# Kernel optimization log

Hardware: AMD Instinct MI355X
Metric: run time of the kernel (lower is better)

Reference implementation:

```python
import jax, jax.numpy as jnp
import numpy as np

B, DIN, H, DOUT = 2048, 1024, 2048, 1024
N_WIDTH, N_ROUTED = 8, 4  # n_layers - 2 = 4 routed expert layers
BN_EPS = 1e-5


def setup_inputs() -> dict:
    key = jax.random.key(0)
    ks = jax.random.split(key, 8)
    # kaiming-normal-ish scales
    x = jax.random.normal(ks[0], (B, DIN), dtype=jnp.float32)
    start_W = jax.random.normal(ks[1], (DIN, H), dtype=jnp.float32) * np.sqrt(2.0 / DIN)
    start_b = jnp.zeros((H,), jnp.float32)
    start_gamma = jnp.ones((H,), jnp.float32)
    start_beta = jnp.zeros((H,), jnp.float32)
    expert_W = jax.random.normal(ks[2], (N_ROUTED, N_WIDTH, H, H), dtype=jnp.float32) * np.sqrt(2.0 / H)
    expert_b = jnp.zeros((N_ROUTED, N_WIDTH, H), jnp.float32)
    bn_gamma = jnp.ones((N_ROUTED, H), jnp.float32)
    bn_beta = jnp.zeros((N_ROUTED, H), jnp.float32)
    dqn_W = jax.random.normal(ks[3], (H, N_WIDTH), dtype=jnp.float32) * np.sqrt(1.0 / H)
    dqn_b = jnp.zeros((N_WIDTH,), jnp.float32)
    end_W = jax.random.normal(ks[4], (H, DOUT), dtype=jnp.float32) * np.sqrt(2.0 / H)
    end_b = jnp.zeros((DOUT,), jnp.float32)
    return {"x": x, "start_W": start_W, "start_b": start_b,
            "start_gamma": start_gamma, "start_beta": start_beta,
            "expert_W": expert_W, "expert_b": expert_b,
            "bn_gamma": bn_gamma, "bn_beta": bn_beta,
            "dqn_W": dqn_W, "dqn_b": dqn_b,
            "end_W": end_W, "end_b": end_b}


def _batchnorm(h, gamma, beta):
    # training-mode BatchNorm1d: biased variance over batch axis
    mu = h.mean(0)
    var = jnp.mean((h - mu) ** 2, axis=0)
    return gamma * (h - mu) * jax.lax.rsqrt(var + BN_EPS) + beta


def reference(x, start_W, start_b, start_gamma, start_beta,
              expert_W, expert_b, bn_gamma, bn_beta,
              dqn_W, dqn_b, end_W, end_b):
    # start: Linear + ReLU + BatchNorm1d
    h = jax.nn.relu(x @ start_W + start_b)            # [B, H]
    h = _batchnorm(h, start_gamma, start_beta)
    # routed expert layers (eval mode: deterministic argmax routing, eps=-1)
    for i in range(N_ROUTED):
        logits = h @ dqn_W + dqn_b                    # [B, E]
        actions = jnp.argmax(logits, axis=1)          # [B]
        onehot = jax.nn.one_hot(actions, N_WIDTH, dtype=h.dtype)  # [B, E]
        # compute all experts densely, then select per-sample expert
        y_all = jax.nn.relu(jnp.einsum('bi,eio->beo', h, expert_W[i]) + expert_b[i][None])  # [B, E, H]
        h = jnp.einsum('beo,be->bo', y_all, onehot)   # [B, H]
        h = _batchnorm(h, bn_gamma[i], bn_beta[i])
    # end: Linear + ReLU
    return jax.nn.relu(h @ end_W + end_b)             # [B, DOUT]
```

## Files before the change

kernel.cpp:

```cpp
#include <hip/hip_runtime.h>
#include <math.h>

#define B_SZ 2048
#define DIN  1024
#define H    2048
#define DOUT 1024
#define NEXP 8
#define NL   4

typedef _Float16 f16;
typedef _Float16 f16x4 __attribute__((ext_vector_type(4)));
typedef _Float16 f16x8 __attribute__((ext_vector_type(8)));
typedef __fp16   h16x2 __attribute__((ext_vector_type(2)));
typedef float    f32x4 __attribute__((ext_vector_type(4)));

#define MFMA16(a,b,c) __builtin_amdgcn_mfma_f32_16x16x32_f16((a),(b),(c),0,0,0)

__global__ __launch_bounds__(256) void k_convert(const float* __restrict__ x,
                                                 f16* __restrict__ hi, f16* __restrict__ lo, int n4){
  int stride = gridDim.x * blockDim.x;
  for (int i = blockIdx.x*blockDim.x + threadIdx.x; i < n4; i += stride){
    float4 v = ((const float4*)x)[i];
    f16 h0=(f16)v.x, h1=(f16)v.y, h2=(f16)v.z, h3=(f16)v.w;
    f16x4 hv = {h0,h1,h2,h3};
    f16x4 lv = {(f16)((v.x-(float)h0)*2048.0f),(f16)((v.y-(float)h1)*2048.0f),
                (f16)((v.z-(float)h2)*2048.0f),(f16)((v.w-(float)h3)*2048.0f)};
    ((f16x4*)hi)[i] = hv;
    ((f16x4*)lo)[i] = lv;
  }
}

template<int PRECISE>
__global__ __launch_bounds__(256, 2) void k_gemm(
    const f16* __restrict__ Ahi, const f16* __restrict__ Alo, int lda,
    const float* __restrict__ Wbase, const float* __restrict__ biasBase,
    int K, int N, int M, int nTx,
    float* __restrict__ Cout, int ldc,
    const int* __restrict__ row_idx, const int* __restrict__ offsets,
    const int* __restrict__ tile_map, const int* __restrict__ ntiles,
    int wStride, int bStride)
{
  const int q = gridDim.x >> 3;
  const int logical = (blockIdx.x & 7) * q + (blockIdx.x >> 3);
  const int ntile_x = logical % nTx;
  const int mtile_l = logical / nTx;

  const bool ident = (tile_map == nullptr);
  int e, mt, roff, cnt;
  if (!ident){
    if (mtile_l >= *ntiles) return;
    int mv = tile_map[mtile_l]; e = mv >> 16; mt = mv & 0xffff;
    roff = offsets[e]; cnt = offsets[e+1] - roff;
  } else { e = 0; mt = mtile_l; roff = 0; cnt = M; }

  const float* W    = Wbase   + (size_t)e * wStride;
  const float* bias = biasBase+ (size_t)e * bStride;
  const int n0   = ntile_x * 128;
  const int tid  = threadIdx.x;
  const int lane = tid & 63;
  const int wid  = tid >> 6;
  const int wm   = (wid >> 1) * 64;
  const int wn   = (wid & 1) * 64;

  __shared__ f16x8 sAh[128*5];
  __shared__ f16x8 sAl[PRECISE ? 128*5 : 1];
  __shared__ f16x8 sBh[128*5];
  __shared__ f16x8 sBl[PRECISE ? 128*5 : 1];

  const int r1 = tid >> 2, sl = tid & 3, r2 = r1 + 64;
  int gr1, gr2;
  {
    int i1 = mt*128 + r1, i2 = mt*128 + r2;
    if (ident){ gr1 = i1; gr2 = i2; }
    else { gr1 = row_idx[roff + (i1 < cnt ? i1 : 0)];
           gr2 = row_idx[roff + (i2 < cnt ? i2 : 0)]; }
  }
  const f16* a1h = Ahi + (size_t)gr1*lda + sl*8;
  const f16* a2h = Ahi + (size_t)gr2*lda + sl*8;
  const f16 *a1l = nullptr, *a2l = nullptr;
  if constexpr (PRECISE){
    a1l = Alo + (size_t)gr1*lda + sl*8;
    a2l = Alo + (size_t)gr2*lda + sl*8;
  }

  const int bn = tid & 127, kb = tid >> 7;
  const float* wp0 = W + (size_t)(kb*16) * N + n0 + bn;

  f32x4 acc0[4][4] = {};
  f32x4 acc1[4][4] = {};

  f16x8 rA1h, rA2h, rA1l, rA2l;
  float rW[16];

  auto issue = [&](int kk){
    rA1h = *(const f16x8*)(a1h + kk);
    rA2h = *(const f16x8*)(a2h + kk);
    if constexpr (PRECISE){
      rA1l = *(const f16x8*)(a1l + kk);
      rA2l = *(const f16x8*)(a2l + kk);
    }
    const float* wp = wp0 + (size_t)kk * N;
    #pragma unroll
    for (int i = 0; i < 16; i++) rW[i] = wp[(size_t)i * N];
  };

  issue(0);

  for (int k0 = 0; k0 < K; k0 += 32){
    sAh[r1*5 + sl] = rA1h;
    sAh[r2*5 + sl] = rA2h;
    if constexpr (PRECISE){
      sAl[r1*5 + sl] = rA1l;
      sAl[r2*5 + sl] = rA2l;
    }
    {
      f16 hs[16], ls[16];
      #pragma unroll
      for (int i = 0; i < 16; i += 2){
        float w0 = rW[i]   * 16.0f;
        float w1 = rW[i+1] * 16.0f;
        h16x2 hp = __builtin_amdgcn_cvt_pkrtz(w0, w1);
        hs[i] = (f16)hp.x; hs[i+1] = (f16)hp.y;
        if constexpr (PRECISE){
          h16x2 lp = __builtin_amdgcn_cvt_pkrtz((w0-(float)hp.x)*2048.0f,
                                                (w1-(float)hp.y)*2048.0f);
          ls[i] = (f16)lp.x; ls[i+1] = (f16)lp.y;
        }
      }
      f16x8 v0 = {hs[0],hs[1],hs[2],hs[3],hs[4],hs[5],hs[6],hs[7]};
      f16x8 v1 = {hs[8],hs[9],hs[10],hs[11],hs[12],hs[13],hs[14],hs[15]};
      sBh[bn*5 + kb*2 + 0] = v0;
      sBh[bn*5 + kb*2 + 1] = v1;
      if constexpr (PRECISE){
        f16x8 u0 = {ls[0],ls[1],ls[2],ls[3],ls[4],ls[5],ls[6],ls[7]};
        f16x8 u1 = {ls[8],ls[9],ls[10],ls[11],ls[12],ls[13],ls[14],ls[15]};
        sBl[bn*5 + kb*2 + 0] = u0;
        sBl[bn*5 + kb*2 + 1] = u1;
      }
    }
    __syncthreads();

    if (k0 + 32 < K) issue(k0 + 32);

    f16x8 ah[4], al[4];
    #pragma unroll
    for (int mf = 0; mf < 4; mf++){
      int row = wm + mf*16 + (lane & 15);
      ah[mf] = sAh[row*5 + (lane >> 4)];
      if constexpr (PRECISE) al[mf] = sAl[row*5 + (lane >> 4)];
    }
    #pragma unroll
    for (int nf = 0; nf < 4; nf++){
      int col = wn + nf*16 + (lane & 15);
      f16x8 bh = sBh[col*5 + (lane >> 4)];
      f16x8 bl;
      if constexpr (PRECISE) bl = sBl[col*5 + (lane >> 4)];
      #pragma unroll
      for (int mf = 0; mf < 4; mf++){
        acc0[mf][nf] = MFMA16(ah[mf], bh, acc0[mf][nf]);
        if constexpr (PRECISE){
          acc1[mf][nf] = MFMA16(ah[mf], bl, acc1[mf][nf]);
          acc1[mf][nf] = MFMA16(al[mf], bh, acc1[mf][nf]);
        }
      }
    }
    __syncthreads();
  }

  const float s1 = 1.0f/16.0f, s2 = 1.0f/(16.0f*2048.0f);
  float bvs[4];
  #pragma unroll
  for (int nf = 0; nf < 4; nf++) bvs[nf] = bias[n0 + wn + nf*16 + (lane & 15)];
  #pragma unroll
  for (int mf = 0; mf < 4; mf++){
    #pragma unroll
    for (int j = 0; j < 4; j++){
      int rt   = wm + mf*16 + (lane >> 4)*4 + j;
      int ridx = mt*128 + rt;
      int gr; bool valid;
      if (ident){ gr = ridx; valid = true; }
      else { valid = (ridx < cnt); gr = valid ? row_idx[roff + ridx] : 0; }
      if (valid){
        float* cp = Cout + (size_t)gr*ldc + n0 + wn + (lane & 15);
        #pragma unroll
        for (int nf = 0; nf < 4; nf++){
          float v = acc0[mf][nf][j]*s1 + bvs[nf];
          if constexpr (PRECISE) v += acc1[mf][nf][j]*s2;
          v = v > 0.0f ? v : 0.0f;
          cp[nf*16] = v;
        }
      }
    }
  }
}

__global__ __launch_bounds__(256) void k_stats(const float* __restrict__ P,
                                               float* __restrict__ psum, float* __restrict__ psq){
  int c  = blockIdx.x*64 + (threadIdx.x & 63);
  int rs = threadIdx.x >> 6;
  int r0 = blockIdx.y * 256;
  float s = 0.f, q = 0.f;
  for (int r = r0 + rs; r < r0 + 256; r += 4){
    float v = P[(size_t)r*H + c]; s += v; q += v*v;
  }
  __shared__ float ls[4][64], lq[4][64];
  ls[rs][threadIdx.x & 63] = s; lq[rs][threadIdx.x & 63] = q;
  __syncthreads();
  if (threadIdx.x < 64){
    int cc = threadIdx.x;
    float S = ls[0][cc]+ls[1][cc]+ls[2][cc]+ls[3][cc];
    float Q = lq[0][cc]+lq[1][cc]+lq[2][cc]+lq[3][cc];
    psum[(size_t)blockIdx.y*H + blockIdx.x*64 + cc] = S;
    psq [(size_t)blockIdx.y*H + blockIdx.x*64 + cc] = Q;
  }
}

__global__ __launch_bounds__(256) void k_norm(const float* __restrict__ P,
    const float* __restrict__ psum, const float* __restrict__ psq,
    const float* __restrict__ gamma, const float* __restrict__ beta,
    f16* __restrict__ Hhi, f16* __restrict__ Hlo){
  __shared__ float sS[64], sT[64];
  int c0 = blockIdx.x * 64;
  int tid = threadIdx.x;
  if (tid < 64){
    float s = 0.f, q = 0.f;
    #pragma unroll
    for (int j = 0; j < 8; j++){ s += psum[(size_t)j*H + c0 + tid]; q += psq[(size_t)j*H + c0 + tid]; }
    float mu  = s * (1.0f/B_SZ);
    float var = q * (1.0f/B_SZ) - mu*mu; var = var > 0.f ? var : 0.f;
    float r   = 1.0f / sqrtf(var + 1e-5f);
    float g   = gamma[c0 + tid] * r;
    sS[tid] = g; sT[tid] = beta[c0 + tid] - mu*g;
  }
  __syncthreads();
  int cg = (tid & 15) * 4;
  int r0 = blockIdx.y * 256;
  for (int r = r0 + (tid >> 4); r < r0 + 256; r += 16){
    float4 v = *(const float4*)&P[(size_t)r*H + c0 + cg];
    float h0 = v.x*sS[cg]   + sT[cg];
    float h1 = v.y*sS[cg+1] + sT[cg+1];
    float h2 = v.z*sS[cg+2] + sT[cg+2];
    float h3 = v.w*sS[cg+3] + sT[cg+3];
    f16 a0=(f16)h0, a1=(f16)h1, a2=(f16)h2, a3=(f16)h3;
    f16x4 hv = {a0,a1,a2,a3};
    f16x4 lv = {(f16)((h0-(float)a0)*2048.0f),(f16)((h1-(float)a1)*2048.0f),
                (f16)((h2-(float)a2)*2048.0f),(f16)((h3-(float)a3)*2048.0f)};
    *(f16x4*)&Hhi[(size_t)r*H + c0 + cg] = hv;
    *(f16x4*)&Hlo[(size_t)r*H + c0 + cg] = lv;
  }
}

__global__ __launch_bounds__(256) void k_logits(const f16* __restrict__ Hhi, const f16* __restrict__ Hlo,
    const float* __restrict__ dqnW, const float* __restrict__ dqnB, int* __restrict__ actions){
  int row  = blockIdx.x*4 + (threadIdx.x >> 6);
  int lane = threadIdx.x & 63;
  float acc[8] = {0,0,0,0,0,0,0,0};
  const f16* ph = Hhi + (size_t)row*H;
  const f16* pl = Hlo + (size_t)row*H;
  #pragma unroll
  for (int t = 0; t < 4; t++){
    int k = t*512 + lane*8;
    f16x8 h8 = *(const f16x8*)(ph + k);
    f16x8 l8 = *(const f16x8*)(pl + k);
    #pragma unroll
    for (int j = 0; j < 8; j++){
      float h = (float)h8[j] + (float)l8[j]*(1.0f/2048.0f);
      const float* w = dqnW + (size_t)(k+j)*NEXP;
      float4 w0 = *(const float4*)w;
      float4 w1 = *(const float4*)(w+4);
      acc[0] += h*w0.x; acc[1] += h*w0.y; acc[2] += h*w0.z; acc[3] += h*w0.w;
      acc[4] += h*w1.x; acc[5] += h*w1.y; acc[6] += h*w1.z; acc[7] += h*w1.w;
    }
  }
  #pragma unroll
  for (int off = 32; off; off >>= 1){
    #pragma unroll
    for (int e2 = 0; e2 < 8; e2++) acc[e2] += __shfl_down(acc[e2], off);
  }
  if (lane == 0){
    float best = acc[0] + dqnB[0]; int bi = 0;
    #pragma unroll
    for (int e2 = 1; e2 < 8; e2++){ float v = acc[e2] + dqnB[e2]; if (v > best){ best = v; bi = e2; } }
    actions[row] = bi;
  }
}

__global__ __launch_bounds__(256) void k_route(const int* __restrict__ actions, int* __restrict__ offsets,
    int* __restrict__ row_idx, int* __restrict__ tile_map, int* __restrict__ ntiles){
  __shared__ int cnt[8], cur[8];
  int tid = threadIdx.x;
  if (tid < 8) cnt[tid] = 0;
  __syncthreads();
  for (int b = tid; b < B_SZ; b += 256) atomicAdd(&cnt[actions[b]], 1);
  __syncthreads();
  if (tid == 0){
    int o = 0, nt = 0;
    for (int e2 = 0; e2 < 8; e2++){
      offsets[e2] = o; cur[e2] = o;
      int c = cnt[e2];
      int t = (c + 127) >> 7;
      for (int ti = 0; ti < t; ti++) tile_map[nt++] = (e2 << 16) | ti;
      o += c;
    }
    offsets[8] = o;
    *ntiles = nt;
  }
  __syncthreads();
  for (int b = tid; b < B_SZ; b += 256){
    int a = actions[b];
    int p = atomicAdd(&cur[a], 1);
    row_idx[p] = b;
  }
}

extern "C" void kernel_launch(void* const* d_in, const int* in_sizes, int n_in,
                              void* d_out, int out_size, void* d_ws, size_t ws_size,
                              hipStream_t stream){
  const float* x           = (const float*)d_in[0];
  const float* start_W     = (const float*)d_in[1];
  const float* start_b     = (const float*)d_in[2];
  const float* start_gamma = (const float*)d_in[3];
  const float* start_beta  = (const float*)d_in[4];
  const float* expert_W    = (const float*)d_in[5];
  const float* expert_b    = (const float*)d_in[6];
  const float* bn_gamma    = (const float*)d_in[7];
  const float* bn_beta     = (const float*)d_in[8];
  const float* dqn_W       = (const float*)d_in[9];
  const float* dqn_b       = (const float*)d_in[10];
  const float* end_W       = (const float*)d_in[11];
  const float* end_b       = (const float*)d_in[12];
  float* out = (float*)d_out;

  char* ws = (char*)d_ws;
  size_t off = 0;
  auto alloc = [&](size_t bytes){ void* p = ws + off; off += (bytes + 255) & ~(size_t)255; return p; };
  f16*   Hhi     = (f16*)  alloc((size_t)B_SZ*H*2);
  f16*   Hlo     = (f16*)  alloc((size_t)B_SZ*H*2);
  float* Ppre    = (float*)alloc((size_t)B_SZ*H*4);
  float* psum    = (float*)alloc((size_t)8*H*4);
  float* psq     = (float*)alloc((size_t)8*H*4);
  int*   actions = (int*)  alloc(B_SZ*4);
  int*   row_idx = (int*)  alloc(B_SZ*4);
  int*   offsets = (int*)  alloc(16*4);
  int*   tile_map= (int*)  alloc(32*4);
  int*   ntiles  = (int*)  alloc(64);

  k_convert<<<512, 256, 0, stream>>>(x, Hhi, Hlo, B_SZ*DIN/4);
  k_gemm<1><<<(B_SZ/128)*(H/128), 256, 0, stream>>>(
      Hhi, Hlo, DIN, start_W, start_b, DIN, H, B_SZ, H/128, Ppre, H,
      nullptr, nullptr, nullptr, nullptr, 0, 0);
  k_stats<<<dim3(H/64, 8), 256, 0, stream>>>(Ppre, psum, psq);
  k_norm <<<dim3(H/64, 8), 256, 0, stream>>>(Ppre, psum, psq, start_gamma, start_beta, Hhi, Hlo);

  for (int i = 0; i < NL; i++){
    k_logits<<<B_SZ/4, 256, 0, stream>>>(Hhi, Hlo, dqn_W, dqn_b, actions);
    k_route <<<1, 256, 0, stream>>>(actions, offsets, row_idx, tile_map, ntiles);
    const float* Wb = expert_W + (size_t)i*NEXP*H*H;
    const float* bb = expert_b + (size_t)i*NEXP*H;
    if (i < 3)
      k_gemm<1><<<23*(H/128), 256, 0, stream>>>(
          Hhi, Hlo, H, Wb, bb, H, H, B_SZ, H/128, Ppre, H,
          row_idx, offsets, tile_map, ntiles, H*H, H);
    else
      k_gemm<0><<<23*(H/128), 256, 0, stream>>>(
          Hhi, nullptr, H, Wb, bb, H, H, B_SZ, H/128, Ppre, H,
          row_idx, offsets, tile_map, ntiles, H*H, H);
    k_stats<<<dim3(H/64, 8), 256, 0, stream>>>(Ppre, psum, psq);
    k_norm <<<dim3(H/64, 8), 256, 0, stream>>>(Ppre, psum, psq,
        bn_gamma + (size_t)i*H, bn_beta + (size_t)i*H, Hhi, Hlo);
  }

  k_gemm<0><<<(B_SZ/128)*(DOUT/128), 256, 0, stream>>>(
      Hhi, nullptr, H, end_W, end_b, H, DOUT, B_SZ, DOUT/128, out, DOUT,
      nullptr, nullptr, nullptr, nullptr, 0, 0);
}
```

Measured before the change: 742.5 us.

## Double-buffer LDS tiles and deepen weight register prefetch in GEMM

Splits the GEMM main loop into two LDS buffers with two register sets for the fp32 weight tile, so weights are prefetched two k-steps ahead and one barrier per step replaces two. Barriers now wait only on LDS counters, which lets global loads stay in flight across compute. The occupancy hint of 2 blocks per SM is dropped from launch bounds. This doubles LDS use and raises register pressure, which may lower occupancy or cause spills. Correctness relies on K being a multiple of 64 and on the double-buffer ordering of writes against the other buffer's reads.

After: 926.1 us. 1.25x slower.

```diff
diff --git a/kernel.cpp b/kernel.cpp
--- a/kernel.cpp
+++ b/kernel.cpp
@@ -15,6 +15,11 @@
 typedef float    f32x4 __attribute__((ext_vector_type(4)));
 
 #define MFMA16(a,b,c) __builtin_amdgcn_mfma_f32_16x16x32_f16((a),(b),(c),0,0,0)
+
+#define BARRIER_LDS() do { \
+    asm volatile("s_waitcnt lgkmcnt(0)" ::: "memory"); \
+    __builtin_amdgcn_s_barrier(); \
+  } while (0)
 
 __global__ __launch_bounds__(256) void k_convert(const float* __restrict__ x,
                                                  f16* __restrict__ hi, f16* __restrict__ lo, int n4){
@@ -31,7 +36,7 @@
 }
 
 template<int PRECISE>
-__global__ __launch_bounds__(256, 2) void k_gemm(
+__global__ __launch_bounds__(256) void k_gemm(
     const f16* __restrict__ Ahi, const f16* __restrict__ Alo, int lda,
     const float* __restrict__ Wbase, const float* __restrict__ biasBase,
     int K, int N, int M, int nTx,
@@ -62,10 +67,10 @@
   const int wm   = (wid >> 1) * 64;
   const int wn   = (wid & 1) * 64;
 
-  __shared__ f16x8 sAh[128*5];
-  __shared__ f16x8 sAl[PRECISE ? 128*5 : 1];
-  __shared__ f16x8 sBh[128*5];
-  __shared__ f16x8 sBl[PRECISE ? 128*5 : 1];
+  __shared__ f16x8 sAh[2][128*5];
+  __shared__ f16x8 sAl[PRECISE ? 2 : 1][PRECISE ? 128*5 : 1];
+  __shared__ f16x8 sBh[2][128*5];
+  __shared__ f16x8 sBl[PRECISE ? 2 : 1][PRECISE ? 128*5 : 1];
 
   const int r1 = tid >> 2, sl = tid & 3, r2 = r1 + 64;
   int gr1, gr2;
@@ -89,72 +94,69 @@
   f32x4 acc0[4][4] = {};
   f32x4 acc1[4][4] = {};
 
+  float rW0[16], rW1[16];
   f16x8 rA1h, rA2h, rA1l, rA2l;
-  float rW[16];
-
-  auto issue = [&](int kk){
+
+  auto issueW = [&](float* rw, int kk){
+    const float* wp = wp0 + (size_t)kk * N;
+    #pragma unroll
+    for (int i = 0; i < 16; i++) rw[i] = wp[(size_t)i * N];
+  };
+  auto issueA = [&](int kk){
     rA1h = *(const f16x8*)(a1h + kk);
     rA2h = *(const f16x8*)(a2h + kk);
     if constexpr (PRECISE){
       rA1l = *(const f16x8*)(a1l + kk);
       rA2l = *(const f16x8*)(a2l + kk);
     }
-    const float* wp = wp0 + (size_t)kk * N;
-    #pragma unroll
-    for (int i = 0; i < 16; i++) rW[i] = wp[(size_t)i * N];
-  };
-
-  issue(0);
-
-  for (int k0 = 0; k0 < K; k0 += 32){
-    sAh[r1*5 + sl] = rA1h;
-    sAh[r2*5 + sl] = rA2h;
+  };
+  auto writeA = [&](int buf){
+    sAh[buf][r1*5 + sl] = rA1h;
+    sAh[buf][r2*5 + sl] = rA2h;
     if constexpr (PRECISE){
-      sAl[r1*5 + sl] = rA1l;
-      sAl[r2*5 + sl] = rA2l;
-    }
-    {
-      f16 hs[16], ls[16];
-      #pragma unroll
-      for (int i = 0; i < 16; i += 2){
-        float w0 = rW[i]   * 16.0f;
-        float w1 = rW[i+1] * 16.0f;
-        h16x2 hp = __builtin_amdgcn_cvt_pkrtz(w0, w1);
-        hs[i] = (f16)hp.x; hs[i+1] = (f16)hp.y;
-        if constexpr (PRECISE){
-          h16x2 lp = __builtin_amdgcn_cvt_pkrtz((w0-(float)hp.x)*2048.0f,
-                                                (w1-(float)hp.y)*2048.0f);
-          ls[i] = (f16)lp.x; ls[i+1] = (f16)lp.y;
-        }
+      sAl[buf][r1*5 + sl] = rA1l;
+      sAl[buf][r2*5 + sl] = rA2l;
+    }
+  };
+  auto writeB = [&](int buf, const float* rw){
+    f16 hs[16], ls[16];
+    #pragma unroll
+    for (int i = 0; i < 16; i += 2){
+      float w0 = rw[i]   * 16.0f;
+      float w1 = rw[i+1] * 16.0f;
+      h16x2 hp = __builtin_amdgcn_cvt_pkrtz(w0, w1);
+      hs[i] = (f16)hp.x; hs[i+1] = (f16)hp.y;
+      if constexpr (PRECISE){
+        h16x2 lp = __builtin_amdgcn_cvt_pkrtz((w0-(float)hp.x)*2048.0f,
+                                              (w1-(float)hp.y)*2048.0f);
+        ls[i] = (f16)lp.x; ls[i+1] = (f16)lp.y;
       }
-      f16x8 v0 = {hs[0],hs[1],hs[2],hs[3],hs[4],hs[5],hs[6],hs[7]};
-      f16x8 v1 = {hs[8],hs[9],hs[10],hs[11],hs[12],hs[13],hs[14],hs[15]};
-      sBh[bn*5 + kb*2 + 0] = v0;
-      sBh[bn*5 + kb*2 + 1] = v1;
-      if constexpr (PRECISE){
-        f16x8 u0 = {ls[0],ls[1],ls[2],ls[3],ls[4],ls[5],ls[6],ls[7]};
-        f16x8 u1 = {ls[8],ls[9],ls[10],ls[11],ls[12],ls[13],ls[14],ls[15]};
-        sBl[bn*5 + kb*2 + 0] = u0;
-        sBl[bn*5 + kb*2 + 1] = u1;
-      }
-    }
-    __syncthreads();
-
-    if (k0 + 32 < K) issue(k0 + 32);
-
+    }
+    f16x8 v0 = {hs[0],hs[1],hs[2],hs[3],hs[4],hs[5],hs[6],hs[7]};
+    f16x8 v1 = {hs[8],hs[9],hs[10],hs[11],hs[12],hs[13],hs[14],hs[15]};
+    sBh[buf][bn*5 + kb*2 + 0] = v0;
+    sBh[buf][bn*5 + kb*2 + 1] = v1;
+    if constexpr (PRECISE){
+      f16x8 u0 = {ls[0],ls[1],ls[2],ls[3],ls[4],ls[5],ls[6],ls[7]};
+      f16x8 u1 = {ls[8],ls[9],ls[10],ls[11],ls[12],ls[13],ls[14],ls[15]};
+      sBl[buf][bn*5 + kb*2 + 0] = u0;
+      sBl[buf][bn*5 + kb*2 + 1] = u1;
+    }
+  };
+  auto compute = [&](int buf){
     f16x8 ah[4], al[4];
     #pragma unroll
     for (int mf = 0; mf < 4; mf++){
       int row = wm + mf*16 + (lane & 15);
-      ah[mf] = sAh[row*5 + (lane >> 4)];
-      if constexpr (PRECISE) al[mf] = sAl[row*5 + (lane >> 4)];
+      ah[mf] = sAh[buf][row*5 + (lane >> 4)];
+      if constexpr (PRECISE) al[mf] = sAl[buf][row*5 + (lane >> 4)];
     }
     #pragma unroll
     for (int nf = 0; nf < 4; nf++){
       int col = wn + nf*16 + (lane & 15);
-      f16x8 bh = sBh[col*5 + (lane >> 4)];
+      f16x8 bh = sBh[buf][col*5 + (lane >> 4)];
       f16x8 bl;
-      if constexpr (PRECISE) bl = sBl[col*5 + (lane >> 4)];
+      if constexpr (PRECISE) bl = sBl[buf][col*5 + (lane >> 4)];
       #pragma unroll
       for (int mf = 0; mf < 4; mf++){
         acc0[mf][nf] = MFMA16(ah[mf], bh, acc0[mf][nf]);
@@ -164,7 +166,25 @@
         }
       }
     }
-    __syncthreads();
+  };
+
+  issueW(rW0, 0);
+  issueW(rW1, 32);
+  issueA(0);
+
+  for (int k0 = 0; k0 < K; k0 += 64){
+    writeA(0);
+    writeB(0, rW0);
+    issueA(k0 + 32);
+    if (k0 + 64 < K) issueW(rW0, k0 + 64);
+    BARRIER_LDS();
+    compute(0);
+    writeA(1);
+    writeB(1, rW1);
+    if (k0 + 64 < K) issueA(k0 + 64);
+    if (k0 + 96 < K) issueW(rW1, k0 + 96);
+    BARRIER_LDS();
+    compute(1);
   }
 
   const float s1 = 1.0f/16.0f, s2 = 1.0f/(16.0f*2048.0f);
```

## Fuse BatchNorm column statistics into GEMM epilogue via fixed-point atomics

Applied to the files above, without the earlier changes.

Removes the separate k_stats pass. Each GEMM epilogue now accumulates per-column sum and sum of squares, reduces them across lanes, and adds them into global 64-bit integer accumulators with atomics; fixed-point keeps the result deterministic. The accumulators are zeroed in k_convert and k_route, and k_norm reads them directly. This saves one full read of the 2048x2048 pre-activation per layer and five launches, at the cost of atomic traffic, fixed-point rounding, and dropping the occupancy hint from the GEMM launch bounds.

Result: slower. 858.8 us (+15.7%).

```diff
diff --git a/kernel.cpp b/kernel.cpp
--- a/kernel.cpp
+++ b/kernel.cpp
@@ -16,8 +16,16 @@
 
 #define MFMA16(a,b,c) __builtin_amdgcn_mfma_f32_16x16x32_f16((a),(b),(c),0,0,0)
 
+#define S_SCALE 1048576.0f
+#define Q_SCALE 65536.0f
+
 __global__ __launch_bounds__(256) void k_convert(const float* __restrict__ x,
-                                                 f16* __restrict__ hi, f16* __restrict__ lo, int n4){
+                                                 f16* __restrict__ hi, f16* __restrict__ lo, int n4,
+                                                 unsigned long long* __restrict__ psumI,
+                                                 unsigned long long* __restrict__ psqI){
+  if (blockIdx.x == 0){
+    for (int c = threadIdx.x; c < H; c += 256){ psumI[c] = 0ull; psqI[c] = 0ull; }
+  }
   int stride = gridDim.x * blockDim.x;
   for (int i = blockIdx.x*blockDim.x + threadIdx.x; i < n4; i += stride){
     float4 v = ((const float4*)x)[i];
@@ -31,14 +39,15 @@
 }
 
 template<int PRECISE>
-__global__ __launch_bounds__(256, 2) void k_gemm(
+__global__ __launch_bounds__(256) void k_gemm(
     const f16* __restrict__ Ahi, const f16* __restrict__ Alo, int lda,
     const float* __restrict__ Wbase, const float* __restrict__ biasBase,
     int K, int N, int M, int nTx,
     float* __restrict__ Cout, int ldc,
     const int* __restrict__ row_idx, const int* __restrict__ offsets,
     const int* __restrict__ tile_map, const int* __restrict__ ntiles,
-    int wStride, int bStride)
+    int wStride, int bStride,
+    unsigned long long* __restrict__ psumI, unsigned long long* __restrict__ psqI)
 {
   const int q = gridDim.x >> 3;
   const int logical = (blockIdx.x & 7) * q + (blockIdx.x >> 3);
@@ -169,6 +178,8 @@
 
   const float s1 = 1.0f/16.0f, s2 = 1.0f/(16.0f*2048.0f);
   float bvs[4];
+  float csum[4] = {0.f,0.f,0.f,0.f};
+  float csq [4] = {0.f,0.f,0.f,0.f};
   #pragma unroll
   for (int nf = 0; nf < 4; nf++) bvs[nf] = bias[n0 + wn + nf*16 + (lane & 15)];
   #pragma unroll
@@ -188,46 +199,40 @@
           if constexpr (PRECISE) v += acc1[mf][nf][j]*s2;
           v = v > 0.0f ? v : 0.0f;
           cp[nf*16] = v;
+          csum[nf] += v;
+          csq [nf] += v*v;
         }
       }
     }
   }
-}
-
-__global__ __launch_bounds__(256) void k_stats(const float* __restrict__ P,
-                                               float* __restrict__ psum, float* __restrict__ psq){
-  int c  = blockIdx.x*64 + (threadIdx.x & 63);
-  int rs = threadIdx.x >> 6;
-  int r0 = blockIdx.y * 256;
-  float s = 0.f, q = 0.f;
-  for (int r = r0 + rs; r < r0 + 256; r += 4){
-    float v = P[(size_t)r*H + c]; s += v; q += v*v;
-  }
-  __shared__ float ls[4][64], lq[4][64];
-  ls[rs][threadIdx.x & 63] = s; lq[rs][threadIdx.x & 63] = q;
-  __syncthreads();
-  if (threadIdx.x < 64){
-    int cc = threadIdx.x;
-    float S = ls[0][cc]+ls[1][cc]+ls[2][cc]+ls[3][cc];
-    float Q = lq[0][cc]+lq[1][cc]+lq[2][cc]+lq[3][cc];
-    psum[(size_t)blockIdx.y*H + blockIdx.x*64 + cc] = S;
-    psq [(size_t)blockIdx.y*H + blockIdx.x*64 + cc] = Q;
+  if (psumI){
+    #pragma unroll
+    for (int nf = 0; nf < 4; nf++){
+      float sv = csum[nf], qv = csq[nf];
+      sv += __shfl_xor(sv, 16); sv += __shfl_xor(sv, 32);
+      qv += __shfl_xor(qv, 16); qv += __shfl_xor(qv, 32);
+      if ((lane >> 4) == 0){
+        int c = n0 + wn + nf*16 + (lane & 15);
+        atomicAdd(&psumI[c], (unsigned long long)(long long)rintf(sv * S_SCALE));
+        atomicAdd(&psqI [c], (unsigned long long)(long long)rintf(qv * Q_SCALE));
+      }
+    }
   }
 }
 
 __global__ __launch_bounds__(256) void k_norm(const float* __restrict__ P,
-    const float* __restrict__ psum, const float* __restrict__ psq,
+    const unsigned long long* __restrict__ psumI, const unsigned long long* __restrict__ psqI,
     const float* __restrict__ gamma, const float* __restrict__ beta,
     f16* __restrict__ Hhi, f16* __restrict__ Hlo){
   __shared__ float sS[64], sT[64];
   int c0 = blockIdx.x * 64;
   int tid = threadIdx.x;
   if (tid < 64){
-    float s = 0.f, q = 0.f;
-    #pragma unroll
-    for (int j = 0; j < 8; j++){ s += psum[(size_t)j*H + c0 + tid]; q += psq[(size_t)j*H + c0 + tid]; }
-    float mu  = s * (1.0f/B_SZ);
-    float var = q * (1.0f/B_SZ) - mu*mu; var = var > 0.f ? var : 0.f;
+    long long S = (long long)psumI[c0 + tid];
+    long long Q = (long long)psqI [c0 + tid];
+    float mu  = (float)((double)S * (1.0 / ((double)S_SCALE * (double)B_SZ)));
+    float ex2 = (float)((double)Q * (1.0 / ((double)Q_SCALE * (double)B_SZ)));
+    float var = ex2 - mu*mu; var = var > 0.f ? var : 0.f;
     float r   = 1.0f / sqrtf(var + 1e-5f);
     float g   = gamma[c0 + tid] * r;
     sS[tid] = g; sT[tid] = beta[c0 + tid] - mu*g;
@@ -286,9 +291,11 @@
 }
 
 __global__ __launch_bounds__(256) void k_route(const int* __restrict__ actions, int* __restrict__ offsets,
-    int* __restrict__ row_idx, int* __restrict__ tile_map, int* __restrict__ ntiles){
+    int* __restrict__ row_idx, int* __restrict__ tile_map, int* __restrict__ ntiles,
+    unsigned long long* __restrict__ psumI, unsigned long long* __restrict__ psqI){
   __shared__ int cnt[8], cur[8];
   int tid = threadIdx.x;
+  for (int c = tid; c < H; c += 256){ psumI[c] = 0ull; psqI[c] = 0ull; }
   if (tid < 8) cnt[tid] = 0;
   __syncthreads();
   for (int b = tid; b < B_SZ; b += 256) atomicAdd(&cnt[actions[b]], 1);
@@ -337,40 +344,38 @@
   f16*   Hhi     = (f16*)  alloc((size_t)B_SZ*H*2);
   f16*   Hlo     = (f16*)  alloc((size_t)B_SZ*H*2);
   float* Ppre    = (float*)alloc((size_t)B_SZ*H*4);
-  float* psum    = (float*)alloc((size_t)8*H*4);
-  float* psq     = (float*)alloc((size_t)8*H*4);
+  unsigned long long* psumI = (unsigned long long*)alloc((size_t)H*8);
+  unsigned long long* psqI  = (unsigned long long*)alloc((size_t)H*8);
   int*   actions = (int*)  alloc(B_SZ*4);
   int*   row_idx = (int*)  alloc(B_SZ*4);
   int*   offsets = (int*)  alloc(16*4);
   int*   tile_map= (int*)  alloc(32*4);
   int*   ntiles  = (int*)  alloc(64);
 
-  k_convert<<<512, 256, 0, stream>>>(x, Hhi, Hlo, B_SZ*DIN/4);
+  k_convert<<<512, 256, 0, stream>>>(x, Hhi, Hlo, B_SZ*DIN/4, psumI, psqI);
   k_gemm<1><<<(B_SZ/128)*(H/128), 256, 0, stream>>>(
       Hhi, Hlo, DIN, start_W, start_b, DIN, H, B_SZ, H/128, Ppre, H,
-      nullptr, nullptr, nullptr, nullptr, 0, 0);
-  k_stats<<<dim3(H/64, 8), 256, 0, stream>>>(Ppre, psum, psq);
-  k_norm <<<dim3(H/64, 8), 256, 0, stream>>>(Ppre, psum, psq, start_gamma, start_beta, Hhi, Hlo);
+      nullptr, nullptr, nullptr, nullptr, 0, 0, psumI, psqI);
+  k_norm <<<dim3(H/64, 8), 256, 0, stream>>>(Ppre, psumI, psqI, start_gamma, start_beta, Hhi, Hlo);
 
   for (int i = 0; i < NL; i++){
     k_logits<<<B_SZ/4, 256, 0, stream>>>(Hhi, Hlo, dqn_W, dqn_b, actions);
-    k_route <<<1, 256, 0, stream>>>(actions, offsets, row_idx, tile_map, ntiles);
+    k_route <<<1, 256, 0, stream>>>(actions, offsets, row_idx, tile_map, ntiles, psumI, psqI);
     const float* Wb = expert_W + (size_t)i*NEXP*H*H;
     const float* bb = expert_b + (size_t)i*NEXP*H;
     if (i < 3)
       k_gemm<1><<<23*(H/128), 256, 0, stream>>>(
           Hhi, Hlo, H, Wb, bb, H, H, B_SZ, H/128, Ppre, H,
-          row_idx, offsets, tile_map, ntiles, H*H, H);
+          row_idx, offsets, tile_map, ntiles, H*H, H, psumI, psqI);
     else
       k_gemm<0><<<23*(H/128), 256, 0, stream>>>(
           Hhi, nullptr, H, Wb, bb, H, H, B_SZ, H/128, Ppre, H,
-          row_idx, offsets, tile_map, ntiles, H*H, H);
-    k_stats<<<dim3(H/64, 8), 256, 0, stream>>>(Ppre, psum, psq);
-    k_norm <<<dim3(H/64, 8), 256, 0, stream>>>(Ppre, psum, psq,
+          row_idx, offsets, tile_map, ntiles, H*H, H, psumI, psqI);
+    k_norm <<<dim3(H/64, 8), 256, 0, stream>>>(Ppre, psumI, psqI,
         bn_gamma + (size_t)i*H, bn_beta + (size_t)i*H, Hhi, Hlo);
   }
 
   k_gemm<0><<<(B_SZ/128)*(DOUT/128), 256, 0, stream>>>(
       Hhi, nullptr, H, end_W, end_b, H, DOUT, B_SZ, DOUT/128, out, DOUT,
-      nullptr, nullptr, nullptr, nullptr, 0, 0);
-}
+      nullptr, nullptr, nullptr, nullptr, 0, 0, nullptr, nullptr);
+}
```

## Fuse routing logits into BatchNorm kernel via fixed-point atomic accumulation

Applied to the files above, without the earlier changes.

Removes the separate logits kernel: the normalize kernel now computes partial dot products with dqn_W per 64-column slice, reduces them with shuffles, and adds them into per-row 64-bit fixed-point accumulators with atomics. The stats kernel zeroes the accumulators, and the route kernel performs the argmax from them. Fixed-point integer atomics keep the sums deterministic so argmax ties are stable, at the cost of many global atomics and some rounding. The GEMM's launch-bounds occupancy hint is also dropped.

New measurement: 1.111 ms. 1.5x slower.

```diff
diff --git a/kernel.cpp b/kernel.cpp
--- a/kernel.cpp
+++ b/kernel.cpp
@@ -15,6 +15,8 @@
 typedef float    f32x4 __attribute__((ext_vector_type(4)));
 
 #define MFMA16(a,b,c) __builtin_amdgcn_mfma_f32_16x16x32_f16((a),(b),(c),0,0,0)
+
+#define L_SCALE 68719476736.0
 
 __global__ __launch_bounds__(256) void k_convert(const float* __restrict__ x,
                                                  f16* __restrict__ hi, f16* __restrict__ lo, int n4){
@@ -31,7 +33,7 @@
 }
 
 template<int PRECISE>
-__global__ __launch_bounds__(256, 2) void k_gemm(
+__global__ __launch_bounds__(256) void k_gemm(
     const f16* __restrict__ Ahi, const f16* __restrict__ Alo, int lda,
     const float* __restrict__ Wbase, const float* __restrict__ biasBase,
     int K, int N, int M, int nTx,
@@ -195,7 +197,12 @@
 }
 
 __global__ __launch_bounds__(256) void k_stats(const float* __restrict__ P,
-                                               float* __restrict__ psum, float* __restrict__ psq){
+                                               float* __restrict__ psum, float* __restrict__ psq,
+                                               unsigned long long* __restrict__ logitAcc){
+  if (logitAcc && blockIdx.y == 0){
+    int base = blockIdx.x * 512;
+    for (int i = threadIdx.x; i < 512; i += 256) logitAcc[base + i] = 0ull;
+  }
   int c  = blockIdx.x*64 + (threadIdx.x & 63);
   int rs = threadIdx.x >> 6;
   int r0 = blockIdx.y * 256;
@@ -215,10 +222,12 @@
   }
 }
 
+template<int LOGITS>
 __global__ __launch_bounds__(256) void k_norm(const float* __restrict__ P,
     const float* __restrict__ psum, const float* __restrict__ psq,
     const float* __restrict__ gamma, const float* __restrict__ beta,
-    f16* __restrict__ Hhi, f16* __restrict__ Hlo){
+    f16* __restrict__ Hhi, f16* __restrict__ Hlo,
+    const float* __restrict__ dqnW, unsigned long long* __restrict__ logitAcc){
   __shared__ float sS[64], sT[64];
   int c0 = blockIdx.x * 64;
   int tid = threadIdx.x;
@@ -235,6 +244,19 @@
   __syncthreads();
   int cg = (tid & 15) * 4;
   int r0 = blockIdx.y * 256;
+  int lane = tid & 63;
+
+  float wv[4][8];
+  if constexpr (LOGITS){
+    #pragma unroll
+    for (int j = 0; j < 4; j++){
+      float4 a = *(const float4*)&dqnW[(size_t)(c0 + cg + j)*NEXP];
+      float4 b = *(const float4*)&dqnW[(size_t)(c0 + cg + j)*NEXP + 4];
+      wv[j][0]=a.x; wv[j][1]=a.y; wv[j][2]=a.z; wv[j][3]=a.w;
+      wv[j][4]=b.x; wv[j][5]=b.y; wv[j][6]=b.z; wv[j][7]=b.w;
+    }
+  }
+
   for (int r = r0 + (tid >> 4); r < r0 + 256; r += 16){
     float4 v = *(const float4*)&P[(size_t)r*H + c0 + cg];
     float h0 = v.x*sS[cg]   + sT[cg];
@@ -247,51 +269,48 @@
                 (f16)((h2-(float)a2)*2048.0f),(f16)((h3-(float)a3)*2048.0f)};
     *(f16x4*)&Hhi[(size_t)r*H + c0 + cg] = hv;
     *(f16x4*)&Hlo[(size_t)r*H + c0 + cg] = lv;
-  }
-}
-
-__global__ __launch_bounds__(256) void k_logits(const f16* __restrict__ Hhi, const f16* __restrict__ Hlo,
-    const float* __restrict__ dqnW, const float* __restrict__ dqnB, int* __restrict__ actions){
-  int row  = blockIdx.x*4 + (threadIdx.x >> 6);
-  int lane = threadIdx.x & 63;
-  float acc[8] = {0,0,0,0,0,0,0,0};
-  const f16* ph = Hhi + (size_t)row*H;
-  const f16* pl = Hlo + (size_t)row*H;
-  #pragma unroll
-  for (int t = 0; t < 4; t++){
-    int k = t*512 + lane*8;
-    f16x8 h8 = *(const f16x8*)(ph + k);
-    f16x8 l8 = *(const f16x8*)(pl + k);
-    #pragma unroll
-    for (int j = 0; j < 8; j++){
-      float h = (float)h8[j] + (float)l8[j]*(1.0f/2048.0f);
-      const float* w = dqnW + (size_t)(k+j)*NEXP;
-      float4 w0 = *(const float4*)w;
-      float4 w1 = *(const float4*)(w+4);
-      acc[0] += h*w0.x; acc[1] += h*w0.y; acc[2] += h*w0.z; acc[3] += h*w0.w;
-      acc[4] += h*w1.x; acc[5] += h*w1.y; acc[6] += h*w1.z; acc[7] += h*w1.w;
-    }
-  }
-  #pragma unroll
-  for (int off = 32; off; off >>= 1){
-    #pragma unroll
-    for (int e2 = 0; e2 < 8; e2++) acc[e2] += __shfl_down(acc[e2], off);
-  }
-  if (lane == 0){
-    float best = acc[0] + dqnB[0]; int bi = 0;
-    #pragma unroll
-    for (int e2 = 1; e2 < 8; e2++){ float v = acc[e2] + dqnB[e2]; if (v > best){ best = v; bi = e2; } }
-    actions[row] = bi;
-  }
-}
-
-__global__ __launch_bounds__(256) void k_route(const int* __restrict__ actions, int* __restrict__ offsets,
-    int* __restrict__ row_idx, int* __restrict__ tile_map, int* __restrict__ ntiles){
+
+    if constexpr (LOGITS){
+      float pe[8];
+      #pragma unroll
+      for (int e = 0; e < 8; e++){
+        float p = h0*wv[0][e] + h1*wv[1][e] + h2*wv[2][e] + h3*wv[3][e];
+        p += __shfl_xor(p, 1); p += __shfl_xor(p, 2);
+        p += __shfl_xor(p, 4); p += __shfl_xor(p, 8);
+        pe[e] = p;
+      }
+      if ((lane & 15) == 0){
+        unsigned long long* dst = logitAcc + (size_t)r*NEXP;
+        #pragma unroll
+        for (int e = 0; e < 8; e++)
+          atomicAdd(&dst[e], (unsigned long long)(long long)llrint((double)pe[e] * L_SCALE));
+      }
+    }
+  }
+}
+
+__global__ __launch_bounds__(256) void k_route(const unsigned long long* __restrict__ logitAcc,
+    const float* __restrict__ dqnB,
+    int* __restrict__ offsets, int* __restrict__ row_idx,
+    int* __restrict__ tile_map, int* __restrict__ ntiles){
   __shared__ int cnt[8], cur[8];
+  __shared__ long long bq[8];
   int tid = threadIdx.x;
-  if (tid < 8) cnt[tid] = 0;
+  if (tid < 8){ cnt[tid] = 0; bq[tid] = (long long)llrint((double)dqnB[tid] * L_SCALE); }
   __syncthreads();
-  for (int b = tid; b < B_SZ; b += 256) atomicAdd(&cnt[actions[b]], 1);
+  int acts[B_SZ/256];
+  int idx = 0;
+  for (int b = tid; b < B_SZ; b += 256, idx++){
+    const long long* row = (const long long*)logitAcc + (size_t)b*NEXP;
+    long long best = row[0] + bq[0]; int bi = 0;
+    #pragma unroll
+    for (int e2 = 1; e2 < 8; e2++){
+      long long v = row[e2] + bq[e2];
+      if (v > best){ best = v; bi = e2; }
+    }
+    acts[idx] = bi;
+    atomicAdd(&cnt[bi], 1);
+  }
   __syncthreads();
   if (tid == 0){
     int o = 0, nt = 0;
@@ -306,8 +325,9 @@
     *ntiles = nt;
   }
   __syncthreads();
-  for (int b = tid; b < B_SZ; b += 256){
-    int a = actions[b];
+  idx = 0;
+  for (int b = tid; b < B_SZ; b += 256, idx++){
+    int a = acts[idx];
     int p = atomicAdd(&cur[a], 1);
     row_idx[p] = b;
   }
@@ -339,7 +359,7 @@
   float* Ppre    = (float*)alloc((size_t)B_SZ*H*4);
   float* psum    = (float*)alloc((size_t)8*H*4);
   float* psq     = (float*)alloc((size_t)8*H*4);
-  int*   actions = (int*)  alloc(B_SZ*4);
+  unsigned long long* logitAcc = (unsigned long long*)alloc((size_t)B_SZ*NEXP*8);
   int*   row_idx = (int*)  alloc(B_SZ*4);
   int*   offsets = (int*)  alloc(16*4);
   int*   tile_map= (int*)  alloc(32*4);
@@ -349,12 +369,12 @@
   k_gemm<1><<<(B_SZ/128)*(H/128), 256, 0, stream>>>(
       Hhi, Hlo, DIN, start_W, start_b, DIN, H, B_SZ, H/128, Ppre, H,
       nullptr, nullptr, nullptr, nullptr, 0, 0);
-  k_stats<<<dim3(H/64, 8), 256, 0, stream>>>(Ppre, psum, psq);
-  k_norm <<<dim3(H/64, 8), 256, 0, stream>>>(Ppre, psum, psq, start_gamma, start_beta, Hhi, Hlo);
+  k_stats<<<dim3(H/64, 8), 256, 0, stream>>>(Ppre, psum, psq, logitAcc);
+  k_norm<1><<<dim3(H/64, 8), 256, 0, stream>>>(Ppre, psum, psq, start_gamma, start_beta,
+      Hhi, Hlo, dqn_W, logitAcc);
 
   for (int i = 0; i < NL; i++){
-    k_logits<<<B_SZ/4, 256, 0, stream>>>(Hhi, Hlo, dqn_W, dqn_b, actions);
-    k_route <<<1, 256, 0, stream>>>(actions, offsets, row_idx, tile_map, ntiles);
+    k_route<<<1, 256, 0, stream>>>(logitAcc, dqn_b, offsets, row_idx, tile_map, ntiles);
     const float* Wb = expert_W + (size_t)i*NEXP*H*H;
     const float* bb = expert_b + (size_t)i*NEXP*H;
     if (i < 3)
@@ -365,9 +385,14 @@
       k_gemm<0><<<23*(H/128), 256, 0, stream>>>(
           Hhi, nullptr, H, Wb, bb, H, H, B_SZ, H/128, Ppre, H,
           row_idx, offsets, tile_map, ntiles, H*H, H);
-    k_stats<<<dim3(H/64, 8), 256, 0, stream>>>(Ppre, psum, psq);
-    k_norm <<<dim3(H/64, 8), 256, 0, stream>>>(Ppre, psum, psq,
-        bn_gamma + (size_t)i*H, bn_beta + (size_t)i*H, Hhi, Hlo);
+    k_stats<<<dim3(H/64, 8), 256, 0, stream>>>(Ppre, psum, psq,
+        (i < 3) ? logitAcc : nullptr);
+    if (i < 3)
+      k_norm<1><<<dim3(H/64, 8), 256, 0, stream>>>(Ppre, psum, psq,
+          bn_gamma + (size_t)i*H, bn_beta + (size_t)i*H, Hhi, Hlo, dqn_W, logitAcc);
+    else
+      k_norm<0><<<dim3(H/64, 8), 256, 0, stream>>>(Ppre, psum, psq,
+          bn_gamma + (size_t)i*H, bn_beta + (size_t)i*H, Hhi, Hlo, nullptr, nullptr);
   }
 
   k_gemm<0><<<(B_SZ/128)*(DOUT/128), 256, 0, stream>>>(
```
